# Kernel tuning notes

Hardware: AMD Instinct MI355X
Metric: run time of the kernel (lower is better)

Reference implementation:

```python
import jax, jax.numpy as jnp
import numpy as np


def setup_inputs() -> dict:
    key = jax.random.key(0)
    k0, k1, k2, k3, k4 = jax.random.split(key, 5)
    B, N, H, d, kproj = 4, 2048, 8, 32, 256
    queries = jax.random.normal(k0, (B, N, H, d), dtype=jnp.float32)
    keys = jax.random.normal(k1, (B, N, H, d), dtype=jnp.float32)
    values = jax.random.normal(k2, (B, N, H, d), dtype=jnp.float32)
    # Linformer sequence projections [N, k]; scaled so projected K/V keep unit-ish variance
    E_proj = jax.random.normal(k3, (N, kproj), dtype=jnp.float32) * 0.02
    F_proj = jax.random.normal(k4, (N, kproj), dtype=jnp.float32) * 0.02
    return {"queries": queries, "keys": keys, "values": values,
            "E_proj": E_proj, "F_proj": F_proj}


def reference(queries, keys, values, E_proj, F_proj):
    """Hybrid attention of dsfa_former:
      (1) FullAttention with triangular causal mask (manual einsum+softmax)
      (2) LinearAttentionHead: Linformer-style sequence projection of K/V via E/F.
    Dropout is identity (eval). Returns (out_full, out_lin), each [B, N, H, d].
    """
    B, N, H, d = queries.shape
    scale = 1.0 / jnp.sqrt(jnp.asarray(d, queries.dtype))

    # ---- FullAttention (causal) ----
    scores = jnp.einsum('blhe,bshe->bhls', queries, keys)  # [B,H,N,N]
    causal = jnp.triu(jnp.ones((N, N), dtype=bool), k=1)   # True above diag -> masked
    scores = jnp.where(causal, -jnp.inf, scores)
    A = jax.nn.softmax(scale * scores, axis=-1)
    out_full = jnp.einsum('bhls,bshd->blhd', A, values)    # [B,N,H,d]

    # ---- LinearAttentionHead (Linformer, no causal mask since kp != N) ----
    Qb = queries.transpose(0, 2, 1, 3)  # [B,H,N,d]
    Kb = keys.transpose(0, 2, 1, 3)
    Vb = values.transpose(0, 2, 1, 3)
    Kp = jnp.einsum('bhnd,nk->bhkd', Kb, E_proj)           # [B,H,k,d]
    Vp = jnp.einsum('bhnd,nk->bhkd', Vb, F_proj)           # [B,H,k,d]
    s_lin = jnp.einsum('bhnd,bhkd->bhnk', Qb, Kp) * scale  # d_k == d
    P = jax.nn.softmax(s_lin, axis=-1)
    out_lin = jnp.einsum('bhnk,bhkd->bhnd', P, Vp).transpose(0, 2, 1, 3)  # [B,N,H,d]

    return out_full, out_lin
```

## Files before the change

### kernel.cpp

```cpp
#include <hip/hip_runtime.h>
#include <hip/hip_bf16.h>


typedef __bf16 bf16x8 __attribute__((ext_vector_type(8)));
typedef __bf16 bf16x2 __attribute__((ext_vector_type(2)));
typedef float f32x4 __attribute__((ext_vector_type(4)));

union BF8 { uint4 u4; ushort us[8]; bf16x8 b; unsigned u32[4]; };

constexpr int B_ = 4, N_ = 2048, H_ = 8, D_ = 32, KP_ = 256, BH_ = 32;
constexpr float SCL2 = 0.25505654442633533f;
constexpr int NFULL = 1024;
constexpr int CHK = 32 * D_;

__device__ __forceinline__ ushort f2bf(float f) {
  unsigned u = __builtin_bit_cast(unsigned, f);
  return (ushort)((u + 0x7FFFu + ((u >> 16) & 1u)) >> 16);
}
__device__ __forceinline__ unsigned pkbf(float f0, float f1) {
#if __has_builtin(__builtin_amdgcn_cvt_pk_bf16_f32)
  bf16x2 r = __builtin_amdgcn_cvt_pk_bf16_f32(f0, f1);
  return __builtin_bit_cast(unsigned, r);
#else
  unsigned u0 = __builtin_bit_cast(unsigned, f0) + 0x8000u;
  unsigned u1 = __builtin_bit_cast(unsigned, f1) + 0x8000u;
  return __builtin_amdgcn_perm(u1, u0, 0x07060302);
#endif
}
__device__ __forceinline__ float bflo(unsigned u) {
  return __builtin_bit_cast(float, u << 16);
}
__device__ __forceinline__ float bfhi(unsigned u) {
  return __builtin_bit_cast(float, u & 0xFFFF0000u);
}
__device__ __forceinline__ float ex2(float x) {
#if __has_builtin(__builtin_amdgcn_exp2f)
  return __builtin_amdgcn_exp2f(x);
#else
  return exp2f(x);
#endif
}

__device__ __forceinline__ void load8_bf(const float* __restrict__ p,
                                         float scale, BF8& hi) {
  float4 a = *reinterpret_cast<const float4*>(p);
  float4 b = *reinterpret_cast<const float4*>(p + 4);
  float x[8] = {a.x, a.y, a.z, a.w, b.x, b.y, b.z, b.w};
#pragma unroll
  for (int i = 0; i < 8; ++i) hi.us[i] = f2bf(x[i] * scale);
}

__global__ __launch_bounds__(256) void k_prep(const float* __restrict__ K,
                                              const float* __restrict__ V,
                                              const float* __restrict__ E,
                                              const float* __restrict__ F,
                                              ushort* __restrict__ KH,
                                              ushort* __restrict__ Kt,
                                              ushort* __restrict__ Vt,
                                              ushort* __restrict__ Et,
                                              ushort* __restrict__ Ft) {
  __shared__ alignas(16) ushort S[4224];
  const int idx = blockIdx.x;
  const int t = threadIdx.x;
  if (idx < 1024) {
    ushort* Tk = S;
    ushort* Tv = S + 2112;
    const int bh = idx >> 5, b = bh >> 3, h = bh & 7;
    const int n0 = (idx & 31) * 64;
    {
      const int row = t >> 2, e8 = (t & 3) * 8;
      const size_t gbase = ((size_t)(b * N_ + n0 + row) * H_ + h) * D_ + e8;
      float4 k0 = *reinterpret_cast<const float4*>(K + gbase);
      float4 k1 = *reinterpret_cast<const float4*>(K + gbase + 4);
      float4 v0 = *reinterpret_cast<const float4*>(V + gbase);
      float4 v1 = *reinterpret_cast<const float4*>(V + gbase + 4);
      float kk[8] = {k0.x,k0.y,k0.z,k0.w,k1.x,k1.y,k1.z,k1.w};
      float vv[8] = {v0.x,v0.y,v0.z,v0.w,v1.x,v1.y,v1.z,v1.w};
      BF8 xh, vh;
#pragma unroll
      for (int i = 0; i < 4; ++i) {
        xh.u32[i] = pkbf(kk[2 * i], kk[2 * i + 1]);
        vh.u32[i] = pkbf(vv[2 * i], vv[2 * i + 1]);
      }
#pragma unroll
      for (int i = 0; i < 8; ++i) {
        Tk[(e8 + i) * 66 + row] = xh.us[i];
        Tv[(e8 + i) * 66 + row] = vh.us[i];
      }
      *reinterpret_cast<uint4*>(KH + ((size_t)bh * N_ + n0 + row) * D_ + e8) = xh.u4;
    }
    __syncthreads();
    {
      const int e = t >> 3, n8 = (t & 7) * 8;
      BF8 xk, xv;
#pragma unroll
      for (int i = 0; i < 8; ++i) {
        xk.us[i] = Tk[e * 66 + n8 + i];
        xv.us[i] = Tv[e * 66 + n8 + i];
      }
      const size_t ob = ((size_t)bh * D_ + e) * N_ + n0 + n8;
      *reinterpret_cast<uint4*>(Kt + ob) = xk.u4;
      *reinterpret_cast<uint4*>(Vt + ob) = xv.u4;
    }
  } else {
    const int j = idx - 1024;
    const float* src = (j >> 7) ? F : E;
    ushort* dst = (j >> 7) ? Ft : Et;
    const int jj = j & 127;
    const int n0 = (jj & 31) * 64, kp0 = (jj >> 5) * 64;
    ushort* T = S;
    {
      const int n = t >> 2, c16 = (t & 3) * 16;
      const size_t gbase = (size_t)(n0 + n) * KP_ + kp0 + c16;
#pragma unroll
      for (int q = 0; q < 4; ++q) {
        float4 x = *reinterpret_cast<const float4*>(src + gbase + q * 4);
        const unsigned u01 = pkbf(x.x, x.y), u23 = pkbf(x.z, x.w);
        T[(c16 + q * 4 + 0) * 66 + n] = (ushort)u01;
        T[(c16 + q * 4 + 1) * 66 + n] = (ushort)(u01 >> 16);
        T[(c16 + q * 4 + 2) * 66 + n] = (ushort)u23;
        T[(c16 + q * 4 + 3) * 66 + n] = (ushort)(u23 >> 16);
      }
    }
    __syncthreads();
    {
      const int kp = t >> 2, n16 = (t & 3) * 16;
      BF8 x0, x1;
#pragma unroll
      for (int i = 0; i < 8; ++i) {
        x0.us[i] = T[kp * 66 + n16 + i];
        x1.us[i] = T[kp * 66 + n16 + 8 + i];
      }
      const size_t ob = (size_t)(kp0 + kp) * N_ + n0 + n16;
      *reinterpret_cast<uint4*>(dst + ob) = x0.u4;
      *reinterpret_cast<uint4*>(dst + ob + 8) = x1.u4;
    }
  }
}

__global__ __launch_bounds__(512) void k_linproj(const ushort* __restrict__ Et,
                                                 const ushort* __restrict__ Ft,
                                                 const ushort* __restrict__ Kt,
                                                 const ushort* __restrict__ Vt,
                                                 ushort* __restrict__ Kp,
                                                 ushort* __restrict__ Vpt) {
  __shared__ float L[8][64][16];
  const int id = blockIdx.x;
  const int bh = (id & 7) + 8 * ((id >> 3) & 3);
  const int kp16 = (id >> 5) * 16;
  const int t = threadIdx.x;
  const int w = t >> 6, lane = t & 63, quad = lane >> 4, l15 = lane & 15;
  const int nbase = w * (N_ / 8);

  const ushort* eA = Et + (size_t)(kp16 + l15) * N_ + nbase + quad * 8;
  const ushort* fA = Ft + (size_t)(kp16 + l15) * N_ + nbase + quad * 8;
  const ushort* kB0 = Kt + ((size_t)bh * D_ + l15) * N_ + nbase + quad * 8;
  const ushort* kB1 = kB0 + (size_t)16 * N_;
  const ushort* vB0 = Vt + ((size_t)bh * D_ + l15) * N_ + nbase + quad * 8;
  const ushort* vB1 = vB0 + (size_t)16 * N_;

  f32x4 accK0 = {0.f,0.f,0.f,0.f}, accK1 = {0.f,0.f,0.f,0.f};
  f32x4 accV0 = {0.f,0.f,0.f,0.f}, accV1 = {0.f,0.f,0.f,0.f};

  BF8 e0, f0, k00, k10, v00, v10;
  BF8 e1, f1, k01, k11, v01, v11;

#define LPLD(E, F, K0, K1, V0, V1, NO)                                \
  do {                                                                \
    (E).u4 = *reinterpret_cast<const uint4*>(eA + (NO));              \
    (F).u4 = *reinterpret_cast<const uint4*>(fA + (NO));              \
    (K0).u4 = *reinterpret_cast<const uint4*>(kB0 + (NO));            \
    (K1).u4 = *reinterpret_cast<const uint4*>(kB1 + (NO));            \
    (V0).u4 = *reinterpret_cast<const uint4*>(vB0 + (NO));            \
    (V1).u4 = *reinterpret_cast<const uint4*>(vB1 + (NO));            \
  } while (0)
#define LPMM(E, F, K0, K1, V0, V1)                                            \
  do {                                                                        \
    accK0 = __builtin_amdgcn_mfma_f32_16x16x32_bf16((E).b, (K0).b, accK0, 0, 0, 0); \
    accK1 = __builtin_amdgcn_mfma_f32_16x16x32_bf16((E).b, (K1).b, accK1, 0, 0, 0); \
    accV0 = __builtin_amdgcn_mfma_f32_16x16x32_bf16((F).b, (V0).b, accV0, 0, 0, 0); \
    accV1 = __builtin_amdgcn_mfma_f32_16x16x32_bf16((F).b, (V1).b, accV1, 0, 0, 0); \
  } while (0)

  LPLD(e0, f0, k00, k10, v00, v10, 0);
  LPLD(e1, f1, k01, k11, v01, v11, 32);
#pragma unroll
  for (int p = 0; p < 3; ++p) {
    LPMM(e0, f0, k00, k10, v00, v10);
    LPLD(e0, f0, k00, k10, v00, v10, (2 * p + 2) * 32);
    LPMM(e1, f1, k01, k11, v01, v11);
    LPLD(e1, f1, k01, k11, v01, v11, (2 * p + 3) * 32);
  }
  LPMM(e0, f0, k00, k10, v00, v10);
  LPMM(e1, f1, k01, k11, v01, v11);
#undef LPLD
#undef LPMM

#pragma unroll
  for (int r = 0; r < 4; ++r) {
    L[w][lane][r]      = accK0[r];
    L[w][lane][4 + r]  = accK1[r];
    L[w][lane][8 + r]  = accV0[r];
    L[w][lane][12 + r] = accV1[r];
  }
  __syncthreads();
  if (w < 4) {
#pragma unroll
    for (int r = 0; r < 4; ++r) {
      const float v = ((L[0][lane][w * 4 + r] + L[1][lane][w * 4 + r]) +
                       (L[2][lane][w * 4 + r] + L[3][lane][w * 4 + r])) +
                      ((L[4][lane][w * 4 + r] + L[5][lane][w * 4 + r]) +
                       (L[6][lane][w * 4 + r] + L[7][lane][w * 4 + r]));
      const int kp = kp16 + quad * 4 + r;
      if (w == 0)      Kp[((size_t)bh * KP_ + kp) * D_ + l15]       = f2bf(v);
      else if (w == 1) Kp[((size_t)bh * KP_ + kp) * D_ + 16 + l15]  = f2bf(v);
      else if (w == 2) Vpt[((size_t)bh * D_ + l15) * KP_ + kp]      = f2bf(v);
      else             Vpt[((size_t)bh * D_ + 16 + l15) * KP_ + kp] = f2bf(v);
    }
  }
}

__global__ __launch_bounds__(256, 4) void k_attn(const float* __restrict__ Q,
                                                 const ushort* __restrict__ KH,
                                                 const ushort* __restrict__ Vt,
                                                 const ushort* __restrict__ Kp,
                                                 const ushort* __restrict__ Vpt,
                                                 float* __restrict__ out) {
  __shared__ alignas(16) unsigned Op[4][4][64][4];
  __shared__ float Ls[4][4][4][4];
  const int idx = blockIdx.x;
  const int t = threadIdx.x;
  const int w = t >> 6, lane = t & 63;
  const int quad = lane >> 4, l15 = lane & 15;
  const int kperm1 = 8 * (l15 >> 2) + (l15 & 3);
  const f32x4 z = {0.f,0.f,0.f,0.f};

  BF8 ones;
#pragma unroll
  for (int i2 = 0; i2 < 4; ++i2) ones.u32[i2] = 0x3F803F80u;

  if (idx < NFULL) {
    const int bh = (idx & 7) + 8 * ((idx >> 3) & 3);
    const int m = 31 - (idx >> 5);
    const int b = bh >> 3, h = bh & 7;
    const int q0 = 64 * m;

    BF8 qh[4];
#pragma unroll
    for (int tt = 0; tt < 4; ++tt)
      load8_bf(Q + ((size_t)(b * N_ + q0 + 16 * tt + l15) * H_ + h) * D_ + quad * 8,
               SCL2, qh[tt]);

    const ushort* KHl = KH + (size_t)bh * N_ * D_ + (size_t)kperm1 * D_ + quad * 8;
    const ushort* V0l = Vt + ((size_t)bh * D_ + l15) * N_ + quad * 8;
    const ushort* V1l = V0l + (size_t)16 * N_;

    const int nun = 2 * m;
    const int cb = (w * nun) >> 2;
    const int ce = ((w + 1) * nun) >> 2;
    const int nwu = ce - cb;

    f32x4 O0[4], O1[4], LS[4];
#pragma unroll
    for (int tt = 0; tt < 4; ++tt) { O0[tt] = z; O1[tt] = z; LS[tt] = z; }

    BF8 kA1, kA2, vA0, vA1, kB1, kB2, vB0, vB1;

    auto procU = [&](BF8& k1, BF8& k2, BF8& v0, BF8& v1) {
      __builtin_amdgcn_s_setprio(1);
#pragma unroll
      for (int tt = 0; tt < 4; ++tt) {
        f32x4 s1 = __builtin_amdgcn_mfma_f32_16x16x32_bf16(k1.b, qh[tt].b, z, 0, 0, 0);
        f32x4 s2 = __builtin_amdgcn_mfma_f32_16x16x32_bf16(k2.b, qh[tt].b, z, 0, 0, 0);
        float e0 = ex2(s1[0]), e1 = ex2(s1[1]), e2 = ex2(s1[2]), e3 = ex2(s1[3]);
        float e4 = ex2(s2[0]), e5 = ex2(s2[1]), e6 = ex2(s2[2]), e7 = ex2(s2[3]);
        BF8 p;
        p.u32[0] = pkbf(e0, e1); p.u32[1] = pkbf(e2, e3);
        p.u32[2] = pkbf(e4, e5); p.u32[3] = pkbf(e6, e7);
        O0[tt] = __builtin_amdgcn_mfma_f32_16x16x32_bf16(p.b, v0.b, O0[tt], 0, 0, 0);
        O1[tt] = __builtin_amdgcn_mfma_f32_16x16x32_bf16(p.b, v1.b, O1[tt], 0, 0, 0);
        LS[tt] = __builtin_amdgcn_mfma_f32_16x16x32_bf16(p.b, ones.b, LS[tt], 0, 0, 0);
      }
      __builtin_amdgcn_s_setprio(0);
    };
    auto procM = [&](BF8& k1, BF8& k2, BF8& v0, BF8& v1, int ta, bool doUnm) {
      __builtin_amdgcn_s_setprio(1);
#pragma unroll
      for (int d = 0; d < 2; ++d) {
        const int tt = ta + d;
        const int thr = d ? 16 + l15 : l15;
        f32x4 s1 = __builtin_amdgcn_mfma_f32_16x16x32_bf16(k1.b, qh[tt].b, z, 0, 0, 0);
        f32x4 s2 = __builtin_amdgcn_mfma_f32_16x16x32_bf16(k2.b, qh[tt].b, z, 0, 0, 0);
        float e[8];
#pragma unroll
        for (int j = 0; j < 8; ++j) {
          const float sv = (j < 4) ? s1[j] : s2[j - 4];
          e[j] = (8 * quad + j <= thr) ? ex2(sv) : 0.f;
        }
        BF8 p;
        p.u32[0] = pkbf(e[0], e[1]); p.u32[1] = pkbf(e[2], e[3]);
        p.u32[2] = pkbf(e[4], e[5]); p.u32[3] = pkbf(e[6], e[7]);
        O0[tt] = __builtin_amdgcn_mfma_f32_16x16x32_bf16(p.b, v0.b, O0[tt], 0, 0, 0);
        O1[tt] = __builtin_amdgcn_mfma_f32_16x16x32_bf16(p.b, v1.b, O1[tt], 0, 0, 0);
        LS[tt] = __builtin_amdgcn_mfma_f32_16x16x32_bf16(p.b, ones.b, LS[tt], 0, 0, 0);
      }
      if (doUnm) {
#pragma unroll
        for (int tt = 2; tt < 4; ++tt) {
          f32x4 s1 = __builtin_amdgcn_mfma_f32_16x16x32_bf16(k1.b, qh[tt].b, z, 0, 0, 0);
          f32x4 s2 = __builtin_amdgcn_mfma_f32_16x16x32_bf16(k2.b, qh[tt].b, z, 0, 0, 0);
          float e0 = ex2(s1[0]), e1 = ex2(s1[1]), e2 = ex2(s1[2]), e3 = ex2(s1[3]);
          float e4 = ex2(s2[0]), e5 = ex2(s2[1]), e6 = ex2(s2[2]), e7 = ex2(s2[3]);
          BF8 p;
          p.u32[0] = pkbf(e0, e1); p.u32[1] = pkbf(e2, e3);
          p.u32[2] = pkbf(e4, e5); p.u32[3] = pkbf(e6, e7);
          O0[tt] = __builtin_amdgcn_mfma_f32_16x16x32_bf16(p.b, v0.b, O0[tt], 0, 0, 0);
          O1[tt] = __builtin_amdgcn_mfma_f32_16x16x32_bf16(p.b, v1.b, O1[tt], 0, 0, 0);
          LS[tt] = __builtin_amdgcn_mfma_f32_16x16x32_bf16(p.b, ones.b, LS[tt], 0, 0, 0);
        }
      }
      __builtin_amdgcn_s_setprio(0);
    };

    kA1.u4 = *reinterpret_cast<const uint4*>(KHl + (size_t)cb * CHK);
    kA2.u4 = *reinterpret_cast<const uint4*>(KHl + (size_t)cb * CHK + 4 * D_);
    vA0.u4 = *reinterpret_cast<const uint4*>(V0l + cb * 32);
    vA1.u4 = *reinterpret_cast<const uint4*>(V1l + cb * 32);
    kB1.u4 = *reinterpret_cast<const uint4*>(KHl + (size_t)(cb + 1) * CHK);
    kB2.u4 = *reinterpret_cast<const uint4*>(KHl + (size_t)(cb + 1) * CHK + 4 * D_);
    vB0.u4 = *reinterpret_cast<const uint4*>(V0l + (cb + 1) * 32);
    vB1.u4 = *reinterpret_cast<const uint4*>(V1l + (cb + 1) * 32);

    const ushort* pKA = KHl + (size_t)(cb + 2) * CHK;
    const ushort* pKB = KHl + (size_t)(cb + 3) * CHK;
    const ushort* pV0 = V0l + (cb + 2) * 32;
    const ushort* pV1 = V1l + (cb + 2) * 32;

    int i = 0;
    for (; i + 2 <= nwu; i += 2) {
      procU(kA1, kA2, vA0, vA1);
      kA1.u4 = *reinterpret_cast<const uint4*>(pKA);
      kA2.u4 = *reinterpret_cast<const uint4*>(pKA + 4 * D_);
      vA0.u4 = *reinterpret_cast<const uint4*>(pV0);
      vA1.u4 = *reinterpret_cast<const uint4*>(pV1);
      procU(kB1, kB2, vB0, vB1);
      kB1.u4 = *reinterpret_cast<const uint4*>(pKB);
      kB2.u4 = *reinterpret_cast<const uint4*>(pKB + 4 * D_);
      vB0.u4 = *reinterpret_cast<const uint4*>(pV0 + 32);
      vB1.u4 = *reinterpret_cast<const uint4*>(pV1 + 32);
      pKA += 2 * CHK; pKB += 2 * CHK; pV0 += 64; pV1 += 64;
    }
    if (i < nwu) {
      procU(kA1, kA2, vA0, vA1);
      if (w == 3) procM(kB1, kB2, vB0, vB1, 0, true);
    } else if (w == 3) {
      procM(kA1, kA2, vA0, vA1, 0, true);
    }
    if (w == 2) {
      const int c2 = nun + 1;
      kB1.u4 = *reinterpret_cast<const uint4*>(KHl + (size_t)c2 * CHK);
      kB2.u4 = *reinterpret_cast<const uint4*>(KHl + (size_t)c2 * CHK + 4 * D_);
      vB0.u4 = *reinterpret_cast<const uint4*>(V0l + c2 * 32);
      vB1.u4 = *reinterpret_cast<const uint4*>(V1l + c2 * 32);
      procM(kB1, kB2, vB0, vB1, 2, false);
    }

#pragma unroll
    for (int tt = 0; tt < 4; ++tt) {
      uint4 pk;
      pk.x = pkbf(O0[tt][0], O0[tt][1]);
      pk.y = pkbf(O0[tt][2], O0[tt][3]);
      pk.z = pkbf(O1[tt][0], O1[tt][1]);
      pk.w = pkbf(O1[tt][2], O1[tt][3]);
      *reinterpret_cast<uint4*>(Op[w][tt][lane]) = pk;
    }
    if (l15 == 0) {
#pragma unroll
      for (int tt = 0; tt < 4; ++tt)
#pragma unroll
        for (int r = 0; r < 4; ++r) Ls[w][tt][quad][r] = LS[tt][r];
    }
    __syncthreads();
    {
      const int tt = w;
      float iv[4];
#pragma unroll
      for (int r = 0; r < 4; ++r) {
        const float l = Ls[0][tt][quad][r] + Ls[1][tt][quad][r] +
                        Ls[2][tt][quad][r] + Ls[3][tt][quad][r];
        iv[r] = __builtin_amdgcn_rcpf(l);
      }
      float A0[4] = {0.f,0.f,0.f,0.f}, A1[4] = {0.f,0.f,0.f,0.f};
#pragma unroll
      for (int s = 0; s < 4; ++s) {
        const uint4 u = *reinterpret_cast<const uint4*>(Op[s][tt][lane]);
        A0[0] += bflo(u.x); A0[1] += bfhi(u.x);
        A0[2] += bflo(u.y); A0[3] += bfhi(u.y);
        A1[0] += bflo(u.z); A1[1] += bfhi(u.z);
        A1[2] += bflo(u.w); A1[3] += bfhi(u.w);
      }
#pragma unroll
      for (int r = 0; r < 4; ++r) {
        const int q = q0 + 16 * tt + quad * 4 + r;
        const size_t base = ((size_t)(b * N_ + q) * H_ + h) * D_;
        out[base + l15]      = A0[r] * iv[r];
        out[base + 16 + l15] = A1[r] * iv[r];
      }
    }
  } else {
    const int j = idx - NFULL;
    const int bh = (j & 7) + 8 * ((j >> 3) & 3);
    const int b = bh >> 3, h = bh & 7;
    const int q0 = (j >> 5) * 64 + w * 16;
    float* olin = out + (size_t)B_ * N_ * H_ * D_;

    BF8 qh;
    load8_bf(Q + ((size_t)(b * N_ + q0 + l15) * H_ + h) * D_ + quad * 8, SCL2, qh);

    const int kperm2 = kperm1 + 4;
    const ushort* KpHb = Kp + (size_t)bh * KP_ * D_ + quad * 8;
    const ushort* Vp0 = Vpt + ((size_t)bh * D_ + l15) * KP_ + quad * 8;
    const ushort* Vp1 = Vp0 + (size_t)16 * KP_;

    BF8 pg[8];
    f32x4 LSum = z;
    __builtin_amdgcn_s_setprio(1);
#pragma unroll
    for (int g = 0; g < 8; ++g) {
      const int kp0 = g * 32;
      BF8 a1, a2;
      a1.u4 = *reinterpret_cast<const uint4*>(KpHb + (size_t)(kp0 + kperm1) * D_);
      a2.u4 = *reinterpret_cast<const uint4*>(KpHb + (size_t)(kp0 + kperm2) * D_);
      f32x4 s1 = __builtin_amdgcn_mfma_f32_16x16x32_bf16(a1.b, qh.b, z, 0, 0, 0);
      f32x4 s2 = __builtin_amdgcn_mfma_f32_16x16x32_bf16(a2.b, qh.b, z, 0, 0, 0);
      const float e0 = ex2(s1[0]), e1 = ex2(s1[1]), e2 = ex2(s1[2]), e3 = ex2(s1[3]);
      const float e4 = ex2(s2[0]), e5 = ex2(s2[1]), e6 = ex2(s2[2]), e7 = ex2(s2[3]);
      pg[g].u32[0] = pkbf(e0, e1); pg[g].u32[1] = pkbf(e2, e3);
      pg[g].u32[2] = pkbf(e4, e5); pg[g].u32[3] = pkbf(e6, e7);
      LSum = __builtin_amdgcn_mfma_f32_16x16x32_bf16(pg[g].b, ones.b, LSum, 0, 0, 0);
    }

    f32x4 O0 = z, O1 = z;
#pragma unroll
    for (int g = 0; g < 8; ++g) {
      BF8 v0, v1;
      v0.u4 = *reinterpret_cast<const uint4*>(Vp0 + g * 32);
      v1.u4 = *reinterpret_cast<const uint4*>(Vp1 + g * 32);
      O0 = __builtin_amdgcn_mfma_f32_16x16x32_bf16(pg[g].b, v0.b, O0, 0, 0, 0);
      O1 = __builtin_amdgcn_mfma_f32_16x16x32_bf16(pg[g].b, v1.b, O1, 0, 0, 0);
    }
    __builtin_amdgcn_s_setprio(0);

#pragma unroll
    for (int r = 0; r < 4; ++r) {
      const float fr = __builtin_amdgcn_rcpf(LSum[r]);
      const int q = q0 + quad * 4 + r;
      const size_t base = ((size_t)(b * N_ + q) * H_ + h) * D_;
      olin[base + l15]      = O0[r] * fr;
      olin[base + 16 + l15] = O1[r] * fr;
    }
  }
}

extern "C" void kernel_launch(void* const* d_in, const int* in_sizes, int n_in,
                              void* d_out, int out_size, void* d_ws, size_t ws_size,
                              hipStream_t stream) {
  const float* Q = (const float*)d_in[0];
  const float* K = (const float*)d_in[1];
  const float* V = (const float*)d_in[2];
  const float* E = (const float*)d_in[3];
  const float* F = (const float*)d_in[4];
  float* out = (float*)d_out;

  ushort* KH  = (ushort*)d_ws;
  ushort* Kt  = KH + (size_t)BH_ * N_ * D_;
  ushort* Vt  = Kt + (size_t)BH_ * N_ * D_;
  ushort* Et  = Vt + (size_t)BH_ * N_ * D_;
  ushort* Ft  = Et + (size_t)KP_ * N_;
  ushort* Kp  = Ft + (size_t)KP_ * N_;
  ushort* Vpt = Kp + (size_t)BH_ * KP_ * D_;

  k_prep<<<dim3(1280), 256, 0, stream>>>(K, V, E, F, KH, Kt, Vt, Et, Ft);
  k_linproj<<<dim3(512), 512, 0, stream>>>(Et, Ft, Kt, Vt, Kp, Vpt);
  k_attn<<<dim3(NFULL + 1024), 256, 0, stream>>>(Q, KH, Vt, Kp, Vpt, out);
}
```

Measured before the change: 143.2 us.

## Store transposed K/V, E/F and projected V in 32-column chunked tiles

Changes the transposed K, V, E, F and projected-V buffers from long row-major rows of length N (or KP) into blocked tiles of 32 contiguous elements per row within 32-wide sequence chunks. Every consumer (linear projection, full attention, Linformer attention) is updated to the new indexing. The aim is for each MFMA operand fetch of a 16x32 tile to hit one contiguous 1 KB region instead of 16 rows strided by several KB, which should improve cache-line and TLB locality. The risk is that the prep kernel's writes become less contiguous and that the address arithmetic gets a little more complex.

```diff
diff --git a/kernel.cpp b/kernel.cpp
--- a/kernel.cpp
+++ b/kernel.cpp
@@ -98,7 +98,8 @@
         xk.us[i] = Tk[e * 66 + n8 + i];
         xv.us[i] = Tv[e * 66 + n8 + i];
       }
-      const size_t ob = ((size_t)bh * D_ + e) * N_ + n0 + n8;
+      const int c = (n0 + n8) >> 5, k = n8 & 31;
+      const size_t ob = (((size_t)bh * 64 + c) * 32 + e) * 32 + k;
       *reinterpret_cast<uint4*>(Kt + ob) = xk.u4;
       *reinterpret_cast<uint4*>(Vt + ob) = xv.u4;
     }
@@ -131,7 +132,8 @@
         x0.us[i] = T[kp * 66 + n16 + i];
         x1.us[i] = T[kp * 66 + n16 + 8 + i];
       }
-      const size_t ob = (size_t)(kp0 + kp) * N_ + n0 + n16;
+      const int c = (n0 + n16) >> 5, k = n16 & 31;
+      const size_t ob = ((size_t)c * KP_ + kp0 + kp) * 32 + k;
       *reinterpret_cast<uint4*>(dst + ob) = x0.u4;
       *reinterpret_cast<uint4*>(dst + ob + 8) = x1.u4;
     }
@@ -150,14 +152,14 @@
   const int kp16 = (id >> 5) * 16;
   const int t = threadIdx.x;
   const int w = t >> 6, lane = t & 63, quad = lane >> 4, l15 = lane & 15;
-  const int nbase = w * (N_ / 8);
-
-  const ushort* eA = Et + (size_t)(kp16 + l15) * N_ + nbase + quad * 8;
-  const ushort* fA = Ft + (size_t)(kp16 + l15) * N_ + nbase + quad * 8;
-  const ushort* kB0 = Kt + ((size_t)bh * D_ + l15) * N_ + nbase + quad * 8;
-  const ushort* kB1 = kB0 + (size_t)16 * N_;
-  const ushort* vB0 = Vt + ((size_t)bh * D_ + l15) * N_ + nbase + quad * 8;
-  const ushort* vB1 = vB0 + (size_t)16 * N_;
+  const int cbase = w * 8;
+
+  const ushort* eA = Et + ((size_t)cbase * KP_ + kp16 + l15) * 32 + quad * 8;
+  const ushort* fA = Ft + ((size_t)cbase * KP_ + kp16 + l15) * 32 + quad * 8;
+  const ushort* kB0 = Kt + (((size_t)bh * 64 + cbase) * 32 + l15) * 32 + quad * 8;
+  const ushort* kB1 = kB0 + 512;
+  const ushort* vB0 = Vt + (((size_t)bh * 64 + cbase) * 32 + l15) * 32 + quad * 8;
+  const ushort* vB1 = vB0 + 512;
 
   f32x4 accK0 = {0.f,0.f,0.f,0.f}, accK1 = {0.f,0.f,0.f,0.f};
   f32x4 accV0 = {0.f,0.f,0.f,0.f}, accV1 = {0.f,0.f,0.f,0.f};
@@ -165,14 +167,14 @@
   BF8 e0, f0, k00, k10, v00, v10;
   BF8 e1, f1, k01, k11, v01, v11;
 
-#define LPLD(E, F, K0, K1, V0, V1, NO)                                \
-  do {                                                                \
-    (E).u4 = *reinterpret_cast<const uint4*>(eA + (NO));              \
-    (F).u4 = *reinterpret_cast<const uint4*>(fA + (NO));              \
-    (K0).u4 = *reinterpret_cast<const uint4*>(kB0 + (NO));            \
-    (K1).u4 = *reinterpret_cast<const uint4*>(kB1 + (NO));            \
-    (V0).u4 = *reinterpret_cast<const uint4*>(vB0 + (NO));            \
-    (V1).u4 = *reinterpret_cast<const uint4*>(vB1 + (NO));            \
+#define LPLD(E, F, K0, K1, V0, V1, I)                                   \
+  do {                                                                  \
+    (E).u4 = *reinterpret_cast<const uint4*>(eA + (size_t)(I) * (KP_ * 32)); \
+    (F).u4 = *reinterpret_cast<const uint4*>(fA + (size_t)(I) * (KP_ * 32)); \
+    (K0).u4 = *reinterpret_cast<const uint4*>(kB0 + (I) * CHK);         \
+    (K1).u4 = *reinterpret_cast<const uint4*>(kB1 + (I) * CHK);         \
+    (V0).u4 = *reinterpret_cast<const uint4*>(vB0 + (I) * CHK);         \
+    (V1).u4 = *reinterpret_cast<const uint4*>(vB1 + (I) * CHK);         \
   } while (0)
 #define LPMM(E, F, K0, K1, V0, V1)                                            \
   do {                                                                        \
@@ -183,13 +185,13 @@
   } while (0)
 
   LPLD(e0, f0, k00, k10, v00, v10, 0);
-  LPLD(e1, f1, k01, k11, v01, v11, 32);
+  LPLD(e1, f1, k01, k11, v01, v11, 1);
 #pragma unroll
   for (int p = 0; p < 3; ++p) {
     LPMM(e0, f0, k00, k10, v00, v10);
-    LPLD(e0, f0, k00, k10, v00, v10, (2 * p + 2) * 32);
+    LPLD(e0, f0, k00, k10, v00, v10, 2 * p + 2);
     LPMM(e1, f1, k01, k11, v01, v11);
-    LPLD(e1, f1, k01, k11, v01, v11, (2 * p + 3) * 32);
+    LPLD(e1, f1, k01, k11, v01, v11, 2 * p + 3);
   }
   LPMM(e0, f0, k00, k10, v00, v10);
   LPMM(e1, f1, k01, k11, v01, v11);
@@ -214,8 +216,10 @@
       const int kp = kp16 + quad * 4 + r;
       if (w == 0)      Kp[((size_t)bh * KP_ + kp) * D_ + l15]       = f2bf(v);
       else if (w == 1) Kp[((size_t)bh * KP_ + kp) * D_ + 16 + l15]  = f2bf(v);
-      else if (w == 2) Vpt[((size_t)bh * D_ + l15) * KP_ + kp]      = f2bf(v);
-      else             Vpt[((size_t)bh * D_ + 16 + l15) * KP_ + kp] = f2bf(v);
+      else if (w == 2)
+        Vpt[(((size_t)bh * 8 + (kp >> 5)) * 32 + l15) * 32 + (kp & 31)] = f2bf(v);
+      else
+        Vpt[(((size_t)bh * 8 + (kp >> 5)) * 32 + 16 + l15) * 32 + (kp & 31)] = f2bf(v);
     }
   }
 }
@@ -252,8 +256,8 @@
                SCL2, qh[tt]);
 
     const ushort* KHl = KH + (size_t)bh * N_ * D_ + (size_t)kperm1 * D_ + quad * 8;
-    const ushort* V0l = Vt + ((size_t)bh * D_ + l15) * N_ + quad * 8;
-    const ushort* V1l = V0l + (size_t)16 * N_;
+    const ushort* V0l = Vt + (size_t)bh * N_ * D_ + l15 * 32 + quad * 8;
+    const ushort* V1l = V0l + 512;
 
     const int nun = 2 * m;
     const int cb = (w * nun) >> 2;
@@ -324,17 +328,17 @@
 
     kA1.u4 = *reinterpret_cast<const uint4*>(KHl + (size_t)cb * CHK);
     kA2.u4 = *reinterpret_cast<const uint4*>(KHl + (size_t)cb * CHK + 4 * D_);
-    vA0.u4 = *reinterpret_cast<const uint4*>(V0l + cb * 32);
-    vA1.u4 = *reinterpret_cast<const uint4*>(V1l + cb * 32);
+    vA0.u4 = *reinterpret_cast<const uint4*>(V0l + (size_t)cb * CHK);
+    vA1.u4 = *reinterpret_cast<const uint4*>(V1l + (size_t)cb * CHK);
     kB1.u4 = *reinterpret_cast<const uint4*>(KHl + (size_t)(cb + 1) * CHK);
     kB2.u4 = *reinterpret_cast<const uint4*>(KHl + (size_t)(cb + 1) * CHK + 4 * D_);
-    vB0.u4 = *reinterpret_cast<const uint4*>(V0l + (cb + 1) * 32);
-    vB1.u4 = *reinterpret_cast<const uint4*>(V1l + (cb + 1) * 32);
+    vB0.u4 = *reinterpret_cast<const uint4*>(V0l + (size_t)(cb + 1) * CHK);
+    vB1.u4 = *reinterpret_cast<const uint4*>(V1l + (size_t)(cb + 1) * CHK);
 
     const ushort* pKA = KHl + (size_t)(cb + 2) * CHK;
     const ushort* pKB = KHl + (size_t)(cb + 3) * CHK;
-    const ushort* pV0 = V0l + (cb + 2) * 32;
-    const ushort* pV1 = V1l + (cb + 2) * 32;
+    const ushort* pV0 = V0l + (size_t)(cb + 2) * CHK;
+    const ushort* pV1 = V1l + (size_t)(cb + 2) * CHK;
 
     int i = 0;
     for (; i + 2 <= nwu; i += 2) {
@@ -346,9 +350,9 @@
       procU(kB1, kB2, vB0, vB1);
       kB1.u4 = *reinterpret_cast<const uint4*>(pKB);
       kB2.u4 = *reinterpret_cast<const uint4*>(pKB + 4 * D_);
-      vB0.u4 = *reinterpret_cast<const uint4*>(pV0 + 32);
-      vB1.u4 = *reinterpret_cast<const uint4*>(pV1 + 32);
-      pKA += 2 * CHK; pKB += 2 * CHK; pV0 += 64; pV1 += 64;
+      vB0.u4 = *reinterpret_cast<const uint4*>(pV0 + CHK);
+      vB1.u4 = *reinterpret_cast<const uint4*>(pV1 + CHK);
+      pKA += 2 * CHK; pKB += 2 * CHK; pV0 += 2 * CHK; pV1 += 2 * CHK;
     }
     if (i < nwu) {
       procU(kA1, kA2, vA0, vA1);
@@ -360,8 +364,8 @@
       const int c2 = nun + 1;
       kB1.u4 = *reinterpret_cast<const uint4*>(KHl + (size_t)c2 * CHK);
       kB2.u4 = *reinterpret_cast<const uint4*>(KHl + (size_t)c2 * CHK + 4 * D_);
-      vB0.u4 = *reinterpret_cast<const uint4*>(V0l + c2 * 32);
-      vB1.u4 = *reinterpret_cast<const uint4*>(V1l + c2 * 32);
+      vB0.u4 = *reinterpret_cast<const uint4*>(V0l + (size_t)c2 * CHK);
+      vB1.u4 = *reinterpret_cast<const uint4*>(V1l + (size_t)c2 * CHK);
       procM(kB1, kB2, vB0, vB1, 2, false);
     }
 
@@ -419,8 +423,8 @@
 
     const int kperm2 = kperm1 + 4;
     const ushort* KpHb = Kp + (size_t)bh * KP_ * D_ + quad * 8;
-    const ushort* Vp0 = Vpt + ((size_t)bh * D_ + l15) * KP_ + quad * 8;
-    const ushort* Vp1 = Vp0 + (size_t)16 * KP_;
+    const ushort* Vp0 = Vpt + (size_t)bh * KP_ * D_ + l15 * 32 + quad * 8;
+    const ushort* Vp1 = Vp0 + 512;
 
     BF8 pg[8];
     f32x4 LSum = z;
@@ -444,8 +448,8 @@
 #pragma unroll
     for (int g = 0; g < 8; ++g) {
       BF8 v0, v1;
-      v0.u4 = *reinterpret_cast<const uint4*>(Vp0 + g * 32);
-      v1.u4 = *reinterpret_cast<const uint4*>(Vp1 + g * 32);
+      v0.u4 = *reinterpret_cast<const uint4*>(Vp0 + g * CHK);
+      v1.u4 = *reinterpret_cast<const uint4*>(Vp1 + g * CHK);
       O0 = __builtin_amdgcn_mfma_f32_16x16x32_bf16(pg[g].b, v0.b, O0, 0, 0, 0);
       O1 = __builtin_amdgcn_mfma_f32_16x16x32_bf16(pg[g].b, v1.b, O1, 0, 0, 0);
     }
```

After: 125.1 us. 12.6% less time.
